# Performance work log

Measured on AMD Instinct MI355X. Metric: run time of the kernel, lower is better.

Reference implementation:

```python
import jax, jax.numpy as jnp
import numpy as np

B = 128
IN = 256
NLVL = 6
KLVL = 3
CH = 4
C = 4 * CH * CH          # 64 channels per node
OU = 8                   # out_filter_siz_u
OV = 8                   # out_filter_siz_v
NK = 2 ** KLVL           # 8 leaf nodes per axis
W_SCALE = 1.0 / 16.0     # ~1/sqrt(2*2*C) so 7 stacked relu-convs stay numerically sane


def setup_inputs() -> dict:
    key = jax.random.key(0)
    ks = jax.random.split(key, 2 * NLVL + 4)
    fx = IN // 2 ** NLVL  # 4: input patch filter size
    inp = {}
    inp["in_data"] = jax.random.normal(ks[0], (B, IN, IN, 1), jnp.float32)
    inp["in_filter"] = jax.random.normal(ks[1], (fx, fx, 1, C), jnp.float32) * W_SCALE
    inp["in_bias"] = jnp.zeros((C,), jnp.float32)
    i = 2
    for lvl in range(1, NLVL + 1):
        n = 2 ** min(lvl, KLVL)  # node grid: grows to 2^klvl then stays
        inp[f"f{lvl}"] = jax.random.normal(ks[i], (n, n, 2, 2, C, C), jnp.float32) * W_SCALE
        inp[f"b{lvl}"] = jnp.zeros((n, n, C), jnp.float32)
        i += 1
    inp["Wd"] = jax.random.normal(ks[i], (NK, NK, 2, C, OU * OV), jnp.float32) * W_SCALE
    return inp


def _node_conv(x, w, b):
    # x: [Nu,Nv,B,H,W,C]; w: [Nu,Nv,2,2,C,C]; 2x2 stride-2 VALID conv per node
    Nu, Nv, Bn, H, W, Cc = x.shape
    xr = x.reshape(Nu, Nv, Bn, H // 2, 2, W // 2, 2, Cc)
    y = jnp.einsum('uvbhxwyc,uvxyco->uvbhwo', xr, w)
    return jax.nn.relu(y + b[:, :, None, None, None, :])


def _forward(in_data, in_filter, in_bias, fs, bs, Wd):
    Bn = in_data.shape[0]
    fx, fy = in_filter.shape[0], in_filter.shape[1]
    # input interp conv: stride == kernel -> non-overlapping patch GEMM
    xr = in_data[..., 0].reshape(Bn, in_data.shape[1] // fx, fx, in_data.shape[2] // fy, fy)
    x = jax.nn.relu(jnp.einsum('bxpyq,pqc->bxyc', xr, in_filter[:, :, 0, :]) + in_bias)
    x = x[None, None]  # [1,1,B,2^nlvl,2^nlvl,C] node grid
    for lvl in range(1, NLVL + 1):
        if lvl <= KLVL:
            # children (itu,itv) read parent (itu//2, itv//2)
            x = jnp.repeat(jnp.repeat(x, 2, axis=0), 2, axis=1)
        x = _node_conv(x, fs[lvl - 1], bs[lvl - 1])
    feats = x[:, :, :, 0, 0, :]  # [NK,NK,B,C]; spatial is 1x1 at level nlvl
    out = jnp.einsum('uvbc,uvrck->uvbrk', feats, Wd)  # r in {real, imag}
    out = out.reshape(NK, NK, Bn, 2, OU, OV)
    out = jnp.transpose(out, (2, 0, 4, 1, 5, 3))  # [B,itu,ou,itv,ov,2]
    return out.reshape(Bn, NK * OU, NK * OV, 2)


def reference(in_data, in_filter, in_bias, f1, b1, f2, b2, f3, b3, f4, b4, f5, b5, f6, b6, Wd):
    fs = (f1, f2, f3, f4, f5, f6)
    bs = (b1, b2, b3, b4, b5, b6)
    return _forward(in_data, in_filter, in_bias, fs, bs, Wd)
```

## Files before the change

### kernel.cpp

```cpp
#include <hip/hip_runtime.h>
#include <hip/hip_bf16.h>
#include <cstdint>
#include <cstddef>


typedef __attribute__((ext_vector_type(8))) short short8;
typedef __attribute__((ext_vector_type(4))) float f32x4;
typedef unsigned short ushort_t;

static __device__ __forceinline__ float b2f(const __hip_bfloat16 x) {
    return __bfloat162float(x);
}
static __device__ __forceinline__ ushort_t f2bf(float x) {
    __hip_bfloat16 h = __float2bfloat16(x);
    ushort_t u;
    __builtin_memcpy(&u, &h, 2);
    return u;
}
static __device__ __forceinline__ void gl_lds16(const void* g, void* l) {
    __builtin_amdgcn_global_load_lds(
        (const __attribute__((address_space(1))) void*)g,
        (__attribute__((address_space(3))) void*)l, 16, 0, 0);
}
#define WAIT_LGKM0() __builtin_amdgcn_s_waitcnt(0xC07F)
#define WAIT_VM0()   __builtin_amdgcn_s_waitcnt(0x0F70)

__global__ __launch_bounds__(256) void k_prep(
    const uint32_t* __restrict__ in_words,
    const void* f1, const void* f2, const void* f3,
    const void* f4, const void* f5, const void* f6, const void* wdsrc,
    const void* b1, const void* b2, const void* b3,
    const void* b4, const void* b5, const void* b6,
    ushort_t* __restrict__ wbuf, ushort_t* __restrict__ wdbuf,
    float* __restrict__ bbuf, int* __restrict__ flag)
{
    __shared__ int sflag;
    const int t = threadIdx.x;
    if (t < 64) {
        const float v = __uint_as_float(in_words[t]);
        const bool plaus = (v == 0.0f) || (fabsf(v) > 1e-8f && fabsf(v) < 1e4f);
        const unsigned long long m = __ballot(plaus);
        if (t == 0) sflag = (__popcll(m) >= 48) ? 0 : 1;
    }
    __syncthreads();
    const int isbf = sflag;
    const int gid = blockIdx.x * 256 + t;
    if (blockIdx.x == 0 && t == 0) *flag = isbf;

    if (gid >= 648448) return;
    if (gid >= 630784) {
        const int bg = gid - 630784;
        const void* src; int base;
        if      (bg <   256) { src = b1; base = 0;     }
        else if (bg <  1280) { src = b2; base = 256;   }
        else if (bg <  5376) { src = b3; base = 1280;  }
        else if (bg <  9472) { src = b4; base = 5376;  }
        else if (bg < 13568) { src = b5; base = 9472;  }
        else                 { src = b6; base = 13568; }
        const int local = bg - base;
        bbuf[bg] = isbf ? b2f(((const __hip_bfloat16*)src)[local])
                        : ((const float*)src)[local];
        return;
    }
    if (gid >= 565248) {
        const int local = gid - 565248;
        const int lane = local & 63;
        const int slot = (local >> 6) & 15;
        const int site = local >> 10;
        const int ks2 = slot >> 3, nh = slot & 7, q = lane >> 4;
        const int n = nh * 16 + (lane & 15);
        const int r = n >> 6, kk = n & 63;
        const int cbase = ks2 * 32 + q * 8;
        ushort_t pk[8];
        if (isbf) {
            const ushort_t* s = (const ushort_t*)wdsrc;
            #pragma unroll
            for (int j = 0; j < 8; j++)
                pk[j] = s[(((size_t)(site * 2 + r) * 64 + cbase + j) * 64) + kk];
        } else {
            const float* s = (const float*)wdsrc;
            #pragma unroll
            for (int j = 0; j < 8; j++)
                pk[j] = f2bf(s[(((size_t)(site * 2 + r) * 64 + cbase + j) * 64) + kk]);
        }
        *(uint4*)&wdbuf[(size_t)local * 8] = *(uint4*)pk;
        return;
    }
    const void* fsrc; int base;
    if      (gid <   8192) { fsrc = f1; base = 0;      }
    else if (gid <  40960) { fsrc = f2; base = 8192;   }
    else if (gid < 172032) { fsrc = f3; base = 40960;  }
    else if (gid < 303104) { fsrc = f4; base = 172032; }
    else if (gid < 434176) { fsrc = f5; base = 303104; }
    else                   { fsrc = f6; base = 434176; }
    const int local = gid - base;
    const int lane = local & 63;
    const int slot = (local >> 6) & 7;
    const int sitetap = local >> 9;
    const int ks = slot >> 2, nh = slot & 3, q = lane >> 4;
    const int n = (lane & 15) + nh * 16;
    const int kbase = ks * 32 + q * 8;
    ushort_t pk[8];
    if (isbf) {
        const ushort_t* s = (const ushort_t*)fsrc + (size_t)sitetap * 4096;
        #pragma unroll
        for (int j = 0; j < 8; j++) pk[j] = s[(kbase + j) * 64 + n];
    } else {
        const float* s = (const float*)fsrc + (size_t)sitetap * 4096;
        #pragma unroll
        for (int j = 0; j < 8; j++) pk[j] = f2bf(s[(kbase + j) * 64 + n]);
    }
    *(uint4*)&wbuf[(size_t)gid * 8] = *(uint4*)pk;
}

__global__ __launch_bounds__(256) void k_stage0(
    const void* __restrict__ in_data, const void* __restrict__ filt,
    const void* __restrict__ bias, __hip_bfloat16* __restrict__ x0,
    const int* __restrict__ flag, int b_off)
{
    const int isbf = *flag;
    const int blk = blockIdx.x;
    const int X  = blk & 63;
    const int bl = blk >> 6;
    const int bg = bl + b_off;

    __shared__ float sIn[4][256];
    __shared__ float sF[16][64];
    __shared__ float sB[64];

    const int t = threadIdx.x;
    const size_t srow = ((size_t)bg * 256 + (size_t)X * 4) * 256;

    if (isbf) {
        const __hip_bfloat16* src = (const __hip_bfloat16*)in_data + srow;
        #pragma unroll
        for (int i = 0; i < 4; i++) {
            int flat = i * 256 + t;
            int p = flat >> 8, col = flat & 255;
            sIn[p][col] = b2f(src[(size_t)p * 256 + col]);
        }
        const __hip_bfloat16* fsrc = (const __hip_bfloat16*)filt;
        #pragma unroll
        for (int i = 0; i < 4; i++) {
            int flat = i * 256 + t;
            sF[flat >> 6][flat & 63] = b2f(fsrc[flat]);
        }
        if (t < 64) sB[t] = b2f(((const __hip_bfloat16*)bias)[t]);
    } else {
        const float* src = (const float*)in_data + srow;
        const int p = t >> 6, c4 = (t & 63) * 4;
        *(float4*)&sIn[p][c4] = *(const float4*)(src + (size_t)p * 256 + c4);
        const float* fsrc = (const float*)filt;
        #pragma unroll
        for (int i = 0; i < 4; i++) {
            int flat = i * 256 + t;
            sF[flat >> 6][flat & 63] = fsrc[flat];
        }
        if (t < 64) sB[t] = ((const float*)bias)[t];
    }
    __syncthreads();

    const int ty = t >> 4;
    const int tc = t & 15;

    float acc[4][4];
    {
        const float4 bv = *(const float4*)&sB[tc * 4];
        #pragma unroll
        for (int yi = 0; yi < 4; yi++) {
            acc[yi][0] = bv.x; acc[yi][1] = bv.y;
            acc[yi][2] = bv.z; acc[yi][3] = bv.w;
        }
    }

    #pragma unroll
    for (int p = 0; p < 4; p++) {
        float4 rin[4], rf[4];
        #pragma unroll
        for (int yi = 0; yi < 4; yi++)
            rin[yi] = *(const float4*)&sIn[p][ty * 16 + yi * 4];
        #pragma unroll
        for (int q = 0; q < 4; q++)
            rf[q] = *(const float4*)&sF[p * 4 + q][tc * 4];
        #pragma unroll
        for (int yi = 0; yi < 4; yi++) {
            #pragma unroll
            for (int q = 0; q < 4; q++) {
                const float a = ((const float*)&rin[yi])[q];
                acc[yi][0] = fmaf(a, rf[q].x, acc[yi][0]);
                acc[yi][1] = fmaf(a, rf[q].y, acc[yi][1]);
                acc[yi][2] = fmaf(a, rf[q].z, acc[yi][2]);
                acc[yi][3] = fmaf(a, rf[q].w, acc[yi][3]);
            }
        }
    }

    ushort_t* dst = (ushort_t*)(x0 + ((size_t)bl * 64 + X) * 64 * 64);
    #pragma unroll
    for (int yi = 0; yi < 4; yi++) {
        uint2 pk;
        pk.x = (uint32_t)f2bf(fmaxf(acc[yi][0], 0.f))
             | ((uint32_t)f2bf(fmaxf(acc[yi][1], 0.f)) << 16);
        pk.y = (uint32_t)f2bf(fmaxf(acc[yi][2], 0.f))
             | ((uint32_t)f2bf(fmaxf(acc[yi][3], 0.f)) << 16);
        *(uint2*)(dst + (size_t)(ty * 4 + yi) * 64 + tc * 4) = pk;
    }
}

__global__ __launch_bounds__(256) void k_level4(
    const __hip_bfloat16* __restrict__ xin,
    const ushort_t* __restrict__ wbuf,
    const float* __restrict__ bbuf,
    __hip_bfloat16* __restrict__ xout,
    int Nv_out, int HW, int Bc, int mtiles)
{
    __shared__ ushort_t smem[20480];
    __shared__ float sBias[4][64];
    ushort_t* sA = smem;
    ushort_t* sB = smem + 4096;

    int idx = blockIdx.x;
    const int mt = idx % mtiles; idx /= mtiles;
    const int w  = idx % HW; idx /= HW;
    const int h  = idx % HW; idx /= HW;
    const int Nv_in = Nv_out >> 1;
    const int vp = idx % Nv_in;
    const int up = idx / Nv_in;

    const int t = threadIdx.x;
    const int wave = t >> 6, lane = t & 63;
    const int lm = lane & 15, lq = lane >> 4;

    {
        const int ct = t >> 6, o = t & 63;
        const int so_t = (2 * up + (ct >> 1)) * Nv_out + (2 * vp + (ct & 1));
        sBias[ct][o] = bbuf[so_t * 64 + o];
    }

    const int so = (2 * up + (wave >> 1)) * Nv_out + (2 * vp + (wave & 1));
    const int H_in = HW * 2;
    const size_t bstride = (size_t)H_in * H_in * 64;
    const size_t siteb = (size_t)(up * Nv_in + vp) * Bc * bstride;
    const ushort_t* wsite = wbuf + (size_t)so * 4 * 4096;

    const f32x4 zero = {0.f, 0.f, 0.f, 0.f};
    f32x4 acc[4][4];
    #pragma unroll
    for (int i = 0; i < 4; i++)
        #pragma unroll
        for (int j = 0; j < 4; j++) acc[i][j] = zero;

    for (int tap = 0; tap < 4; tap++) {
        const int hi = 2 * h + (tap >> 1), wi = 2 * w + (tap & 1);
        const size_t tapoff = siteb + ((size_t)hi * H_in + wi) * 64;
        #pragma unroll
        for (int s2 = 0; s2 < 2; s2++) {
            const int s = wave * 2 + s2;
            const int ks = s >> 2, mh = s & 3;
            int b = mt * 64 + lm + mh * 16;
            if (b >= Bc) b = Bc - 1;
            gl_lds16(xin + tapoff + (size_t)b * bstride + ks * 32 + lq * 8,
                     &sA[s * 512]);
        }
        const ushort_t* wt = wsite + (size_t)tap * 4096;
        #pragma unroll
        for (int s = 0; s < 8; s++) {
            gl_lds16(wt + s * 512 + lane * 8, &sB[wave * 4096 + s * 512]);
        }
        __syncthreads();

        #pragma unroll
        for (int ks = 0; ks < 2; ks++) {
            short8 bf0 = *(const short8*)&sB[wave * 4096 + (ks * 4 + 0) * 512 + lane * 8];
            short8 bf1 = *(const short8*)&sB[wave * 4096 + (ks * 4 + 1) * 512 + lane * 8];
            short8 bf2 = *(const short8*)&sB[wave * 4096 + (ks * 4 + 2) * 512 + lane * 8];
            short8 bf3 = *(const short8*)&sB[wave * 4096 + (ks * 4 + 3) * 512 + lane * 8];
            #pragma unroll
            for (int fm = 0; fm < 4; fm++) {
                short8 a = *(const short8*)&sA[(ks * 4 + fm) * 512 + lane * 8];
                acc[fm][0] = __builtin_amdgcn_mfma_f32_16x16x32_bf16(a, bf0, acc[fm][0], 0, 0, 0);
                acc[fm][1] = __builtin_amdgcn_mfma_f32_16x16x32_bf16(a, bf1, acc[fm][1], 0, 0, 0);
                acc[fm][2] = __builtin_amdgcn_mfma_f32_16x16x32_bf16(a, bf2, acc[fm][2], 0, 0, 0);
                acc[fm][3] = __builtin_amdgcn_mfma_f32_16x16x32_bf16(a, bf3, acc[fm][3], 0, 0, 0);
            }
        }
        __syncthreads();
    }

    float bv[4];
    #pragma unroll
    for (int fn = 0; fn < 4; fn++) bv[fn] = sBias[wave][fn * 16 + lm];
    ushort_t* so_buf = smem + wave * 4352;
    #pragma unroll
    for (int fm = 0; fm < 4; fm++) {
        #pragma unroll
        for (int fn = 0; fn < 4; fn++) {
            #pragma unroll
            for (int r = 0; r < 4; r++) {
                const int row = fm * 16 + lq * 4 + r;
                so_buf[row * 68 + fn * 16 + lm] =
                    f2bf(fmaxf(acc[fm][fn][r] + bv[fn], 0.f));
            }
        }
    }
    __syncthreads();

    const size_t ostride = (size_t)HW * HW * 64;
    const size_t obase = (size_t)so * Bc * ostride + ((size_t)h * HW + w) * 64;
    #pragma unroll
    for (int i = 0; i < 8; i++) {
        const int task = i * 64 + lane;
        const int oct = task & 7, row = task >> 3;
        const int b = mt * 64 + row;
        if (b < Bc) {
            *(uint4*)(xout + obase + (size_t)b * ostride + oct * 8) =
                *(const uint4*)&so_buf[row * 68 + oct * 8];
        }
    }
}

__global__ __launch_bounds__(256, 1) void k_f456(
    const __hip_bfloat16* __restrict__ xin,
    const ushort_t* __restrict__ w4, const ushort_t* __restrict__ w5,
    const ushort_t* __restrict__ w6, const ushort_t* __restrict__ wd,
    const float* __restrict__ b4, const float* __restrict__ b5,
    const float* __restrict__ b6,
    void* __restrict__ out, const int* __restrict__ flag,
    int Bc, int b_off, int mtiles)
{
    const int isbf = *flag;
    const int bx = blockIdx.x;
    const int mt = bx % mtiles;
    const int site = bx / mtiles;
    const int u = site >> 3, v = site & 7;

    __shared__ ushort_t smem[74752];
    __shared__ float sBias[192];

    const int t = threadIdx.x;
    const int wv = t >> 6, lane = t & 63;
    const int lm = lane & 15, lq = lane >> 4;

    if (t < 64) {
        sBias[t]       = b4[site * 64 + t];
        sBias[64 + t]  = b5[site * 64 + t];
        sBias[128 + t] = b6[site * 64 + t];
    }

    {
        const ushort_t* w4s = w4 + (size_t)site * 16384;
        const ushort_t* w5s = w5 + (size_t)site * 16384;
        #pragma unroll
        for (int s2 = 0; s2 < 8; s2++) {
            const int s = wv * 8 + s2;
            gl_lds16(w4s + s * 512 + lane * 8, &smem[s * 512]);
            gl_lds16(w5s + s * 512 + lane * 8, &smem[16384 + s * 512]);
        }
    }
    __syncthreads();

    const f32x4 zero = {0.f, 0.f, 0.f, 0.f};
    const int h5 = wv >> 1, w5p = wv & 1;
    ushort_t* mid1w = smem + 32768 + wv * 8448;
    ushort_t* Aw = smem + 66560 + wv * 2048;
    const size_t sb = (size_t)site * Bc;

    for (int i = 0; i < 4; i++) {
        const int h4 = 2 * h5 + (i >> 1), w4p = 2 * w5p + (i & 1);
        f32x4 acc[2][4];
        #pragma unroll
        for (int a_ = 0; a_ < 2; a_++)
            #pragma unroll
            for (int b_ = 0; b_ < 4; b_++) acc[a_][b_] = zero;

        for (int tap = 0; tap < 4; tap++) {
            const int h3 = 2 * h4 + (tap >> 1), w3 = 2 * w4p + (tap & 1);
            WAIT_LGKM0();
            #pragma unroll
            for (int sl = 0; sl < 4; sl++) {
                const int ks = sl >> 1, mh = sl & 1;
                int b = mt * 32 + mh * 16 + lm;
                if (b >= Bc) b = Bc - 1;
                gl_lds16(xin + (sb + b) * 4096 + (h3 * 8 + w3) * 64 + ks * 32 + lq * 8,
                         &Aw[sl * 512]);
            }
            WAIT_VM0();
            #pragma unroll
            for (int ks = 0; ks < 2; ks++) {
                #pragma unroll
                for (int fm = 0; fm < 2; fm++) {
                    short8 a = *(const short8*)&Aw[(ks * 2 + fm) * 512 + lane * 8];
                    #pragma unroll
                    for (int fn = 0; fn < 4; fn++) {
                        short8 bfr = *(const short8*)&smem[(tap * 8 + ks * 4 + fn) * 512 + lane * 8];
                        acc[fm][fn] = __builtin_amdgcn_mfma_f32_16x16x32_bf16(a, bfr, acc[fm][fn], 0, 0, 0);
                    }
                }
            }
        }
        #pragma unroll
        for (int fm = 0; fm < 2; fm++) {
            #pragma unroll
            for (int fn = 0; fn < 4; fn++) {
                #pragma unroll
                for (int r = 0; r < 4; r++) {
                    const int m = fm * 16 + lq * 4 + r;
                    const int ch = fn * 16 + lm;
                    mid1w[m * 264 + i * 64 + ch] =
                        f2bf(fmaxf(acc[fm][fn][r] + sBias[ch], 0.f));
                }
            }
        }
    }

    {
        f32x4 acc2[2][4];
        #pragma unroll
        for (int a_ = 0; a_ < 2; a_++)
            #pragma unroll
            for (int b_ = 0; b_ < 4; b_++) acc2[a_][b_] = zero;

        #pragma unroll
        for (int i = 0; i < 4; i++) {
            #pragma unroll
            for (int ks = 0; ks < 2; ks++) {
                short8 a0 = *(const short8*)&mid1w[lm * 264 + i * 64 + ks * 32 + lq * 8];
                short8 a1 = *(const short8*)&mid1w[(16 + lm) * 264 + i * 64 + ks * 32 + lq * 8];
                #pragma unroll
                for (int fn = 0; fn < 4; fn++) {
                    short8 bfr = *(const short8*)&smem[16384 + (i * 8 + ks * 4 + fn) * 512 + lane * 8];
                    acc2[0][fn] = __builtin_amdgcn_mfma_f32_16x16x32_bf16(a0, bfr, acc2[0][fn], 0, 0, 0);
                    acc2[1][fn] = __builtin_amdgcn_mfma_f32_16x16x32_bf16(a1, bfr, acc2[1][fn], 0, 0, 0);
                }
            }
        }
        #pragma unroll
        for (int fm = 0; fm < 2; fm++) {
            #pragma unroll
            for (int fn = 0; fn < 4; fn++) {
                #pragma unroll
                for (int r = 0; r < 4; r++) {
                    const int m = fm * 16 + lq * 4 + r;
                    const int ch = fn * 16 + lm;
                    mid1w[m * 72 + ch] =
                        f2bf(fmaxf(acc2[fm][fn][r] + sBias[64 + ch], 0.f));
                }
            }
        }
    }
    __syncthreads();

    {
        const ushort_t* w6s = w6 + (size_t)site * 16384;
        const ushort_t* wds = wd + (size_t)site * 8192;
        #pragma unroll
        for (int s2 = 0; s2 < 8; s2++) {
            const int s = wv * 8 + s2;
            gl_lds16(w6s + s * 512 + lane * 8, &smem[s * 512]);
        }
        #pragma unroll
        for (int s2 = 0; s2 < 4; s2++) {
            const int s = wv * 4 + s2;
            gl_lds16(wds + s * 512 + lane * 8, &smem[16384 + s * 512]);
        }
    }
    __syncthreads();

    {
        f32x4 acc3[2];
        acc3[0] = zero; acc3[1] = zero;
        #pragma unroll
        for (int tap = 0; tap < 4; tap++) {
            const ushort_t* sl = smem + 32768 + tap * 8448;
            #pragma unroll
            for (int ks = 0; ks < 2; ks++) {
                short8 a0 = *(const short8*)&sl[lm * 72 + ks * 32 + lq * 8];
                short8 a1 = *(const short8*)&sl[(16 + lm) * 72 + ks * 32 + lq * 8];
                short8 bfr = *(const short8*)&smem[(tap * 8 + ks * 4 + wv) * 512 + lane * 8];
                acc3[0] = __builtin_amdgcn_mfma_f32_16x16x32_bf16(a0, bfr, acc3[0], 0, 0, 0);
                acc3[1] = __builtin_amdgcn_mfma_f32_16x16x32_bf16(a1, bfr, acc3[1], 0, 0, 0);
            }
        }
        ushort_t* mid3 = smem + 66560;
        #pragma unroll
        for (int fm = 0; fm < 2; fm++) {
            #pragma unroll
            for (int r = 0; r < 4; r++) {
                const int m = fm * 16 + lq * 4 + r;
                const int ch = wv * 16 + lm;
                mid3[m * 72 + ch] =
                    f2bf(fmaxf(acc3[fm][r] + sBias[128 + ch], 0.f));
            }
        }
    }
    __syncthreads();

    {
        const ushort_t* mid3 = smem + 66560;
        f32x4 acc4[2][2];
        acc4[0][0] = zero; acc4[0][1] = zero; acc4[1][0] = zero; acc4[1][1] = zero;
        #pragma unroll
        for (int ks = 0; ks < 2; ks++) {
            short8 a0 = *(const short8*)&mid3[lm * 72 + ks * 32 + lq * 8];
            short8 a1 = *(const short8*)&mid3[(16 + lm) * 72 + ks * 32 + lq * 8];
            #pragma unroll
            for (int n2 = 0; n2 < 2; n2++) {
                const int nh = 2 * wv + n2;
                short8 bfr = *(const short8*)&smem[16384 + (ks * 8 + nh) * 512 + lane * 8];
                acc4[0][n2] = __builtin_amdgcn_mfma_f32_16x16x32_bf16(a0, bfr, acc4[0][n2], 0, 0, 0);
                acc4[1][n2] = __builtin_amdgcn_mfma_f32_16x16x32_bf16(a1, bfr, acc4[1][n2], 0, 0, 0);
            }
        }
        #pragma unroll
        for (int fm = 0; fm < 2; fm++) {
            #pragma unroll
            for (int n2 = 0; n2 < 2; n2++) {
                const int n = (2 * wv + n2) * 16 + lm;
                const int rr = n >> 6, ou = (n >> 3) & 7, ov = n & 7;
                const size_t obase =
                    (((size_t)(u * 8 + ou)) * 64 + (v * 8 + ov)) * 2 + rr;
                #pragma unroll
                for (int reg = 0; reg < 4; reg++) {
                    const int brow = mt * 32 + fm * 16 + lq * 4 + reg;
                    if (brow < Bc) {
                        const size_t oidx = obase + (size_t)(b_off + brow) * 8192;
                        if (isbf) ((__hip_bfloat16*)out)[oidx] =
                            __float2bfloat16(acc4[fm][n2][reg]);
                        else ((float*)out)[oidx] = acc4[fm][n2][reg];
                    }
                }
            }
        }
    }
}

extern "C" void kernel_launch(void* const* d_in, const int* in_sizes, int n_in,
                              void* d_out, int out_size, void* d_ws, size_t ws_size,
                              hipStream_t stream)
{
    (void)in_sizes; (void)n_in; (void)out_size;

    const void* in_data = d_in[0];
    const void* filt    = d_in[1];
    const void* bias0   = d_in[2];
    const void* fl[7];
    const void* bl[7];
    for (int l = 1; l <= 6; l++) {
        fl[l] = d_in[1 + 2 * l];
        bl[l] = d_in[2 + 2 * l];
    }
    const void* Wd = d_in[15];

    const int Bfull = 128;
    const size_t perB = (size_t)64 * 64 * 64;

    const size_t wbufBytes  = 565248ull * 16;
    const size_t wdbufBytes = 65536ull * 16;
    const size_t bbufBytes  = 17664ull * 4;
    const size_t headBytes  = 256 + wbufBytes + wdbufBytes + bbufBytes;

    const size_t avail = ws_size > headBytes ? ws_size - headBytes : 0;
    int Bc = 0;
    for (int c = 128; c >= 1; c >>= 1) {
        if ((size_t)2 * c * perB * sizeof(__hip_bfloat16) <= avail) { Bc = c; break; }
    }
    if (Bc == 0) return;

    int* flag = (int*)d_ws;
    ushort_t* wbuf  = (ushort_t*)((char*)d_ws + 256);
    ushort_t* wdbuf = (ushort_t*)((char*)d_ws + 256 + wbufBytes);
    float* bbuf = (float*)((char*)d_ws + 256 + wbufBytes + wdbufBytes);
    __hip_bfloat16* bufA = (__hip_bfloat16*)((char*)d_ws + headBytes);
    __hip_bfloat16* bufB = bufA + (size_t)Bc * perB;

    static const size_t w_off[7] = {0, 0, 65536, 327680, 1376256, 2424832, 3473408};
    static const int    b_off_tab[7] = {0, 0, 256, 1280, 5376, 9472, 13568};

    k_prep<<<dim3(2533), 256, 0, stream>>>(
        (const uint32_t*)in_data,
        fl[1], fl[2], fl[3], fl[4], fl[5], fl[6], Wd,
        bl[1], bl[2], bl[3], bl[4], bl[5], bl[6],
        wbuf, wdbuf, bbuf, flag);

    const int mt4 = (Bc + 63) / 64;
    const int mt32 = (Bc + 31) / 32;

    for (int b_off = 0; b_off < Bfull; b_off += Bc) {
        k_stage0<<<dim3(Bc * 64), 256, 0, stream>>>(in_data, filt, bias0, bufA, flag, b_off);

        __hip_bfloat16* cur = bufA;
        __hip_bfloat16* nxt = bufB;
        for (int lvl = 1; lvl <= 3; lvl++) {
            const int Nu = 1 << lvl;
            const int H  = 64 >> lvl;
            const int Nv_in = Nu >> 1;
            dim3 grid(Nv_in * Nv_in * H * H * mt4);
            k_level4<<<grid, 256, 0, stream>>>(cur, wbuf + w_off[lvl],
                bbuf + b_off_tab[lvl], nxt, Nu, H, Bc, mt4);
            __hip_bfloat16* tmp = cur; cur = nxt; nxt = tmp;
        }

        k_f456<<<dim3(64 * mt32), 256, 0, stream>>>(cur,
            wbuf + w_off[4], wbuf + w_off[5], wbuf + w_off[6], wdbuf,
            bbuf + b_off_tab[4], bbuf + b_off_tab[5], bbuf + b_off_tab[6],
            d_out, flag, Bc, b_off, mt32);
    }
}
```

Before: 248.8 us.

## Fuse input patch conv with level-1 node conv into one kernel

Replaces the separate stage-0 kernel and the first level-1 launch with a single kernel. It computes the input patch convolution for a 2x2 neighbourhood of 32 batch items in registers, writes the bf16 result straight into LDS in MFMA fragment layout, then runs the level-1 2x2 conv with MFMA against weights streamed into LDS. This removes the global write and re-read of the large stage-0 activation buffer and one launch, at the cost of more LDS per block and recomputing the FP32 patch GEMM per tile.

```diff
diff --git a/kernel.cpp b/kernel.cpp
--- a/kernel.cpp
+++ b/kernel.cpp
@@ -113,97 +113,169 @@
     *(uint4*)&wbuf[(size_t)gid * 8] = *(uint4*)pk;
 }
 
-__global__ __launch_bounds__(256) void k_stage0(
-    const void* __restrict__ in_data, const void* __restrict__ filt,
-    const void* __restrict__ bias, __hip_bfloat16* __restrict__ x0,
-    const int* __restrict__ flag, int b_off)
+__global__ __launch_bounds__(256, 2) void k_s01(
+    const void* __restrict__ in_data,
+    const void* __restrict__ filt,
+    const void* __restrict__ bias0,
+    const ushort_t* __restrict__ w1,
+    const float* __restrict__ b1,
+    __hip_bfloat16* __restrict__ xout,
+    const int* __restrict__ flag, int Bc, int b_off, int mtiles)
 {
     const int isbf = *flag;
-    const int blk = blockIdx.x;
-    const int X  = blk & 63;
-    const int bl = blk >> 6;
-    const int bg = bl + b_off;
-
-    __shared__ float sIn[4][256];
+    int idx = blockIdx.x;
+    const int mt = idx % mtiles; idx /= mtiles;
+    const int w = idx & 31;
+    const int h = idx >> 5;
+
+    __shared__ float sIn[32][64];
     __shared__ float sF[16][64];
-    __shared__ float sB[64];
+    __shared__ float sB0[64];
+    __shared__ float sBias[4][64];
+    __shared__ ushort_t sA[4 * 4 * 512];
+    __shared__ ushort_t sB[4 * 8 * 512];
 
     const int t = threadIdx.x;
-    const size_t srow = ((size_t)bg * 256 + (size_t)X * 4) * 256;
+    const int wave = t >> 6, lane = t & 63;
+    const int lm = lane & 15, lq = lane >> 4;
 
     if (isbf) {
-        const __hip_bfloat16* src = (const __hip_bfloat16*)in_data + srow;
-        #pragma unroll
-        for (int i = 0; i < 4; i++) {
-            int flat = i * 256 + t;
-            int p = flat >> 8, col = flat & 255;
-            sIn[p][col] = b2f(src[(size_t)p * 256 + col]);
-        }
         const __hip_bfloat16* fsrc = (const __hip_bfloat16*)filt;
         #pragma unroll
         for (int i = 0; i < 4; i++) {
             int flat = i * 256 + t;
             sF[flat >> 6][flat & 63] = b2f(fsrc[flat]);
         }
-        if (t < 64) sB[t] = b2f(((const __hip_bfloat16*)bias)[t]);
+        if (t < 64) sB0[t] = b2f(((const __hip_bfloat16*)bias0)[t]);
     } else {
-        const float* src = (const float*)in_data + srow;
-        const int p = t >> 6, c4 = (t & 63) * 4;
-        *(float4*)&sIn[p][c4] = *(const float4*)(src + (size_t)p * 256 + c4);
         const float* fsrc = (const float*)filt;
         #pragma unroll
         for (int i = 0; i < 4; i++) {
             int flat = i * 256 + t;
             sF[flat >> 6][flat & 63] = fsrc[flat];
         }
-        if (t < 64) sB[t] = ((const float*)bias)[t];
-    }
-    __syncthreads();
-
-    const int ty = t >> 4;
-    const int tc = t & 15;
-
-    float acc[4][4];
-    {
-        const float4 bv = *(const float4*)&sB[tc * 4];
-        #pragma unroll
-        for (int yi = 0; yi < 4; yi++) {
-            acc[yi][0] = bv.x; acc[yi][1] = bv.y;
-            acc[yi][2] = bv.z; acc[yi][3] = bv.w;
-        }
-    }
+        if (t < 64) sB0[t] = ((const float*)bias0)[t];
+    }
+    sBias[t >> 6][t & 63] = b1[(t >> 6) * 64 + (t & 63)];
 
     #pragma unroll
-    for (int p = 0; p < 4; p++) {
-        float4 rin[4], rf[4];
-        #pragma unroll
-        for (int yi = 0; yi < 4; yi++)
-            rin[yi] = *(const float4*)&sIn[p][ty * 16 + yi * 4];
-        #pragma unroll
-        for (int q = 0; q < 4; q++)
-            rf[q] = *(const float4*)&sF[p * 4 + q][tc * 4];
-        #pragma unroll
-        for (int yi = 0; yi < 4; yi++) {
-            #pragma unroll
-            for (int q = 0; q < 4; q++) {
-                const float a = ((const float*)&rin[yi])[q];
-                acc[yi][0] = fmaf(a, rf[q].x, acc[yi][0]);
-                acc[yi][1] = fmaf(a, rf[q].y, acc[yi][1]);
-                acc[yi][2] = fmaf(a, rf[q].z, acc[yi][2]);
-                acc[yi][3] = fmaf(a, rf[q].w, acc[yi][3]);
-            }
-        }
-    }
-
-    ushort_t* dst = (ushort_t*)(x0 + ((size_t)bl * 64 + X) * 64 * 64);
+    for (int i = 0; i < 2; i++) {
+        const int task = i * 256 + t;
+        const int half = task & 1, r = (task >> 1) & 7, b = task >> 4;
+        int bl = mt * 32 + b;
+        if (bl >= Bc) bl = Bc - 1;
+        const size_t off = ((size_t)(b_off + bl) * 256 + 8 * h + r) * 256
+                         + 8 * w + half * 4;
+        float4 val;
+        if (isbf) {
+            const __hip_bfloat16* s = (const __hip_bfloat16*)in_data + off;
+            val.x = b2f(s[0]); val.y = b2f(s[1]); val.z = b2f(s[2]); val.w = b2f(s[3]);
+        } else {
+            val = *(const float4*)((const float*)in_data + off);
+        }
+        *(float4*)&sIn[b][r * 8 + half * 4] = val;
+    }
+    __syncthreads();
+
+    {
+        const int vb = t >> 3, oct = t & 7;
+        float4 pf[16][2];
+        #pragma unroll
+        for (int pq = 0; pq < 16; pq++) {
+            pf[pq][0] = *(const float4*)&sF[pq][oct * 8];
+            pf[pq][1] = *(const float4*)&sF[pq][oct * 8 + 4];
+        }
+        const int ks = oct >> 2;
+        const int slot = ks * 2 + (vb >> 4);
+        const int ln = (vb & 15) | ((oct & 3) << 4);
+        #pragma unroll
+        for (int tap = 0; tap < 4; tap++) {
+            const int x = tap >> 1, y = tap & 1;
+            float4 rin[4];
+            #pragma unroll
+            for (int p = 0; p < 4; p++)
+                rin[p] = *(const float4*)&sIn[vb][(4 * x + p) * 8 + 4 * y];
+            float acc8[8];
+            #pragma unroll
+            for (int j = 0; j < 8; j++) acc8[j] = sB0[oct * 8 + j];
+            #pragma unroll
+            for (int p = 0; p < 4; p++) {
+                #pragma unroll
+                for (int q = 0; q < 4; q++) {
+                    const float a = ((const float*)&rin[p])[q];
+                    const float* fp = (const float*)&pf[p * 4 + q][0];
+                    #pragma unroll
+                    for (int j = 0; j < 8; j++)
+                        acc8[j] = fmaf(a, fp[j], acc8[j]);
+                }
+            }
+            ushort_t pk[8];
+            #pragma unroll
+            for (int j = 0; j < 8; j++) pk[j] = f2bf(fmaxf(acc8[j], 0.f));
+            *(uint4*)&sA[((tap * 4 + slot) * 64 + ln) * 8] = *(uint4*)pk;
+        }
+    }
+    __syncthreads();
+
+    const f32x4 zero = {0.f, 0.f, 0.f, 0.f};
+    f32x4 accm[2][4];
     #pragma unroll
-    for (int yi = 0; yi < 4; yi++) {
-        uint2 pk;
-        pk.x = (uint32_t)f2bf(fmaxf(acc[yi][0], 0.f))
-             | ((uint32_t)f2bf(fmaxf(acc[yi][1], 0.f)) << 16);
-        pk.y = (uint32_t)f2bf(fmaxf(acc[yi][2], 0.f))
-             | ((uint32_t)f2bf(fmaxf(acc[yi][3], 0.f)) << 16);
-        *(uint2*)(dst + (size_t)(ty * 4 + yi) * 64 + tc * 4) = pk;
+    for (int i = 0; i < 2; i++)
+        #pragma unroll
+        for (int j = 0; j < 4; j++) accm[i][j] = zero;
+
+    const ushort_t* wsite = w1 + (size_t)wave * 4 * 4096;
+    for (int tap = 0; tap < 4; tap++) {
+        WAIT_LGKM0();
+        const ushort_t* wt = wsite + (size_t)tap * 4096;
+        #pragma unroll
+        for (int s = 0; s < 8; s++)
+            gl_lds16(wt + s * 512 + lane * 8, &sB[wave * 4096 + s * 512]);
+        WAIT_VM0();
+        #pragma unroll
+        for (int ks = 0; ks < 2; ks++) {
+            #pragma unroll
+            for (int fm = 0; fm < 2; fm++) {
+                short8 a = *(const short8*)&sA[((tap * 4 + ks * 2 + fm) * 64 + lane) * 8];
+                #pragma unroll
+                for (int fn = 0; fn < 4; fn++) {
+                    short8 bfr = *(const short8*)&sB[wave * 4096 + (ks * 4 + fn) * 512 + lane * 8];
+                    accm[fm][fn] = __builtin_amdgcn_mfma_f32_16x16x32_bf16(a, bfr, accm[fm][fn], 0, 0, 0);
+                }
+            }
+        }
+    }
+
+    WAIT_LGKM0();
+    {
+        float bv[4];
+        #pragma unroll
+        for (int fn = 0; fn < 4; fn++) bv[fn] = sBias[wave][fn * 16 + lm];
+        ushort_t* ob = &sB[wave * 4096];
+        #pragma unroll
+        for (int fm = 0; fm < 2; fm++) {
+            #pragma unroll
+            for (int fn = 0; fn < 4; fn++) {
+                #pragma unroll
+                for (int r = 0; r < 4; r++) {
+                    const int row = fm * 16 + lq * 4 + r;
+                    ob[row * 68 + fn * 16 + lm] =
+                        f2bf(fmaxf(accm[fm][fn][r] + bv[fn], 0.f));
+                }
+            }
+        }
+        const size_t ostride = (size_t)32 * 32 * 64;
+        const size_t obase = (size_t)wave * Bc * ostride + ((size_t)h * 32 + w) * 64;
+        #pragma unroll
+        for (int i = 0; i < 4; i++) {
+            const int task = i * 64 + lane;
+            const int oc = task & 7, row = task >> 3;
+            const int b = mt * 32 + row;
+            if (b < Bc) {
+                *(uint4*)(xout + obase + (size_t)b * ostride + oc * 8) =
+                    *(const uint4*)&ob[row * 68 + oc * 8];
+            }
+        }
     }
 }
 
@@ -586,11 +658,13 @@
     const int mt32 = (Bc + 31) / 32;
 
     for (int b_off = 0; b_off < Bfull; b_off += Bc) {
-        k_stage0<<<dim3(Bc * 64), 256, 0, stream>>>(in_data, filt, bias0, bufA, flag, b_off);
+        k_s01<<<dim3(1024 * mt32), 256, 0, stream>>>(
+            in_data, filt, bias0, wbuf + w_off[1], bbuf + b_off_tab[1],
+            bufA, flag, Bc, b_off, mt32);
 
         __hip_bfloat16* cur = bufA;
         __hip_bfloat16* nxt = bufB;
-        for (int lvl = 1; lvl <= 3; lvl++) {
+        for (int lvl = 2; lvl <= 3; lvl++) {
             const int Nu = 1 << lvl;
             const int H  = 64 >> lvl;
             const int Nv_in = Nu >> 1;
```

Result: slower. 271.5 us (+9.1%).

## Fuse tree levels 2 and 3 into one kernel via LDS intermediate

Applied to the files above, without the earlier changes.

Adds a kernel that computes level-2 node convolutions for four sibling nodes and immediately feeds the results, held in shared memory, into the level-3 convolutions. The level-2 activation no longer makes a round trip through global memory, and one launch is removed per batch chunk. The cost is that each block recomputes for a 32-batch tile using up to four waves, with a different grid decomposition and occupancy target, which may lower MFMA efficiency or occupancy compared with the generic level kernel.

```diff
diff --git a/kernel.cpp b/kernel.cpp
--- a/kernel.cpp
+++ b/kernel.cpp
@@ -319,6 +319,169 @@
     }
 }
 
+__global__ __launch_bounds__(256, 4) void k_L23(
+    const __hip_bfloat16* __restrict__ xin,
+    const ushort_t* __restrict__ w2buf,
+    const ushort_t* __restrict__ w3buf,
+    const float* __restrict__ b2, const float* __restrict__ b3,
+    __hip_bfloat16* __restrict__ xout,
+    int Bc, int mtiles)
+{
+    __shared__ ushort_t smem[17408];
+    __shared__ float sBias2[64];
+    __shared__ float sBias3[4][64];
+
+    int idx = blockIdx.x;
+    const int sib = idx & 3; idx >>= 2;
+    const int mt = idx % mtiles; idx /= mtiles;
+    const int hw = idx & 63; idx >>= 6;
+    const int s1 = idx;
+    const int h3 = hw >> 3, w3 = hw & 7;
+    const int u2 = 2 * (s1 >> 1) + (sib >> 1);
+    const int v2 = 2 * (s1 & 1) + (sib & 1);
+    const int s2 = u2 * 4 + v2;
+
+    const int t = threadIdx.x;
+    const int wv = t >> 6, lane = t & 63;
+    const int lm = lane & 15, lq = lane >> 4;
+
+    {
+        const int ct = t >> 6, o = t & 63;
+        const int s3t = (2 * u2 + (ct >> 1)) * 8 + 2 * v2 + (ct & 1);
+        sBias3[ct][o] = b3[s3t * 64 + o];
+        if (t < 64) sBias2[t] = b2[s2 * 64 + t];
+    }
+    __syncthreads();
+
+    const f32x4 zero = {0.f, 0.f, 0.f, 0.f};
+    ushort_t* Aw = smem + wv * 2048;
+    ushort_t* midw = smem + 8192 + wv * 2304;
+
+    {
+        const int h2 = 2 * h3 + (wv >> 1), w2p = 2 * w3 + (wv & 1);
+        const size_t a1base = (size_t)s1 * Bc * 65536;
+        const ushort_t* w2site = w2buf + (size_t)s2 * 16384;
+
+        f32x4 acc[2][4];
+        #pragma unroll
+        for (int a_ = 0; a_ < 2; a_++)
+            #pragma unroll
+            for (int b_ = 0; b_ < 4; b_++) acc[a_][b_] = zero;
+
+        for (int tap = 0; tap < 4; tap++) {
+            const int hi = 2 * h2 + (tap >> 1), wi = 2 * w2p + (tap & 1);
+            WAIT_LGKM0();
+            #pragma unroll
+            for (int sl = 0; sl < 4; sl++) {
+                const int ks = sl >> 1, mh = sl & 1;
+                int b = mt * 32 + mh * 16 + lm;
+                if (b >= Bc) b = Bc - 1;
+                gl_lds16(xin + a1base + (size_t)b * 65536
+                             + ((size_t)hi * 32 + wi) * 64 + ks * 32 + lq * 8,
+                         &Aw[sl * 512]);
+            }
+            short8 bfr[2][4];
+            #pragma unroll
+            for (int ks = 0; ks < 2; ks++)
+                #pragma unroll
+                for (int fn = 0; fn < 4; fn++)
+                    bfr[ks][fn] = *(const short8*)(w2site + (size_t)tap * 4096
+                                                   + (ks * 4 + fn) * 512 + lane * 8);
+            WAIT_VM0();
+            #pragma unroll
+            for (int ks = 0; ks < 2; ks++) {
+                #pragma unroll
+                for (int fm = 0; fm < 2; fm++) {
+                    short8 a = *(const short8*)&Aw[(ks * 2 + fm) * 512 + lane * 8];
+                    #pragma unroll
+                    for (int fn = 0; fn < 4; fn++)
+                        acc[fm][fn] = __builtin_amdgcn_mfma_f32_16x16x32_bf16(
+                            a, bfr[ks][fn], acc[fm][fn], 0, 0, 0);
+                }
+            }
+        }
+        #pragma unroll
+        for (int fm = 0; fm < 2; fm++) {
+            #pragma unroll
+            for (int fn = 0; fn < 4; fn++) {
+                #pragma unroll
+                for (int r = 0; r < 4; r++) {
+                    const int m = fm * 16 + lq * 4 + r;
+                    const int ch = fn * 16 + lm;
+                    midw[m * 72 + ch] =
+                        f2bf(fmaxf(acc[fm][fn][r] + sBias2[ch], 0.f));
+                }
+            }
+        }
+    }
+    __syncthreads();
+
+    f32x4 acc3[2][4];
+    #pragma unroll
+    for (int a_ = 0; a_ < 2; a_++)
+        #pragma unroll
+        for (int b_ = 0; b_ < 4; b_++) acc3[a_][b_] = zero;
+
+    const int u3 = 2 * u2 + (wv >> 1), v3 = 2 * v2 + (wv & 1);
+    const int s3 = u3 * 8 + v3;
+    {
+        const ushort_t* w3site = w3buf + (size_t)s3 * 16384;
+        for (int tap = 0; tap < 4; tap++) {
+            const ushort_t* sl = smem + 8192 + tap * 2304;
+            short8 bfr[2][4];
+            #pragma unroll
+            for (int ks = 0; ks < 2; ks++)
+                #pragma unroll
+                for (int fn = 0; fn < 4; fn++)
+                    bfr[ks][fn] = *(const short8*)(w3site + (size_t)tap * 4096
+                                                   + (ks * 4 + fn) * 512 + lane * 8);
+            #pragma unroll
+            for (int ks = 0; ks < 2; ks++) {
+                short8 a0 = *(const short8*)&sl[lm * 72 + ks * 32 + lq * 8];
+                short8 a1 = *(const short8*)&sl[(16 + lm) * 72 + ks * 32 + lq * 8];
+                #pragma unroll
+                for (int fn = 0; fn < 4; fn++) {
+                    acc3[0][fn] = __builtin_amdgcn_mfma_f32_16x16x32_bf16(
+                        a0, bfr[ks][fn], acc3[0][fn], 0, 0, 0);
+                    acc3[1][fn] = __builtin_amdgcn_mfma_f32_16x16x32_bf16(
+                        a1, bfr[ks][fn], acc3[1][fn], 0, 0, 0);
+                }
+            }
+        }
+    }
+    __syncthreads();
+
+    {
+        float bv[4];
+        #pragma unroll
+        for (int fn = 0; fn < 4; fn++) bv[fn] = sBias3[wv][fn * 16 + lm];
+        ushort_t* epi = midw;
+        #pragma unroll
+        for (int fm = 0; fm < 2; fm++) {
+            #pragma unroll
+            for (int fn = 0; fn < 4; fn++) {
+                #pragma unroll
+                for (int r = 0; r < 4; r++) {
+                    const int row = fm * 16 + lq * 4 + r;
+                    epi[row * 68 + fn * 16 + lm] =
+                        f2bf(fmaxf(acc3[fm][fn][r] + bv[fn], 0.f));
+                }
+            }
+        }
+        const size_t obase = (size_t)s3 * Bc * 4096 + ((size_t)h3 * 8 + w3) * 64;
+        #pragma unroll
+        for (int i = 0; i < 4; i++) {
+            const int task = i * 64 + lane;
+            const int oc = task & 7, row = task >> 3;
+            const int b = mt * 32 + row;
+            if (b < Bc) {
+                *(uint4*)(xout + obase + (size_t)b * 4096 + oc * 8) =
+                    *(const uint4*)&epi[row * 68 + oc * 8];
+            }
+        }
+    }
+}
+
 __global__ __launch_bounds__(256, 1) void k_f456(
     const __hip_bfloat16* __restrict__ xin,
     const ushort_t* __restrict__ w4, const ushort_t* __restrict__ w5,
@@ -588,19 +751,14 @@
     for (int b_off = 0; b_off < Bfull; b_off += Bc) {
         k_stage0<<<dim3(Bc * 64), 256, 0, stream>>>(in_data, filt, bias0, bufA, flag, b_off);
 
-        __hip_bfloat16* cur = bufA;
-        __hip_bfloat16* nxt = bufB;
-        for (int lvl = 1; lvl <= 3; lvl++) {
-            const int Nu = 1 << lvl;
-            const int H  = 64 >> lvl;
-            const int Nv_in = Nu >> 1;
-            dim3 grid(Nv_in * Nv_in * H * H * mt4);
-            k_level4<<<grid, 256, 0, stream>>>(cur, wbuf + w_off[lvl],
-                bbuf + b_off_tab[lvl], nxt, Nu, H, Bc, mt4);
-            __hip_bfloat16* tmp = cur; cur = nxt; nxt = tmp;
-        }
-
-        k_f456<<<dim3(64 * mt32), 256, 0, stream>>>(cur,
+        k_level4<<<dim3(32 * 32 * mt4), 256, 0, stream>>>(
+            bufA, wbuf + w_off[1], bbuf + b_off_tab[1], bufB, 2, 32, Bc, mt4);
+
+        k_L23<<<dim3(1024 * mt32), 256, 0, stream>>>(
+            bufB, wbuf + w_off[2], wbuf + w_off[3],
+            bbuf + b_off_tab[2], bbuf + b_off_tab[3], bufA, Bc, mt32);
+
+        k_f456<<<dim3(64 * mt32), 256, 0, stream>>>(bufA,
             wbuf + w_off[4], wbuf + w_off[5], wbuf + w_off[6], wdbuf,
             bbuf + b_off_tab[4], bbuf + b_off_tab[5], bbuf + b_off_tab[6],
             d_out, flag, Bc, b_off, mt32);
```

After: 259.3 us. 4.2% more time.

## Double-buffer activation tiles and load weights directly to registers in level-4 kernel

Applied to the files above, without the earlier changes.

The level-4 node conv kernel now keeps two activation buffers in LDS. It prefetches the next tap's activations while the MFMAs for the current tap run, and needs one barrier per tap instead of two. Weight fragments are read straight from global memory into registers instead of being staged through LDS, which also shrinks the shared memory footprint. In exchange, global weight loads now sit on the critical path of each tap, and register pressure goes up.

```diff
diff --git a/kernel.cpp b/kernel.cpp
--- a/kernel.cpp
+++ b/kernel.cpp
@@ -214,10 +214,8 @@
     __hip_bfloat16* __restrict__ xout,
     int Nv_out, int HW, int Bc, int mtiles)
 {
-    __shared__ ushort_t smem[20480];
+    __shared__ ushort_t smem[17408];
     __shared__ float sBias[4][64];
-    ushort_t* sA = smem;
-    ushort_t* sB = smem + 4096;
 
     int idx = blockIdx.x;
     const int mt = idx % mtiles; idx /= mtiles;
@@ -243,6 +241,15 @@
     const size_t siteb = (size_t)(up * Nv_in + vp) * Bc * bstride;
     const ushort_t* wsite = wbuf + (size_t)so * 4 * 4096;
 
+    int arow[2];
+    #pragma unroll
+    for (int s2 = 0; s2 < 2; s2++) {
+        const int s = wave * 2 + s2;
+        int b = mt * 64 + lm + (s & 3) * 16;
+        if (b >= Bc) b = Bc - 1;
+        arow[s2] = b;
+    }
+
     const f32x4 zero = {0.f, 0.f, 0.f, 0.f};
     f32x4 acc[4][4];
     #pragma unroll
@@ -250,41 +257,51 @@
         #pragma unroll
         for (int j = 0; j < 4; j++) acc[i][j] = zero;
 
-    for (int tap = 0; tap < 4; tap++) {
-        const int hi = 2 * h + (tap >> 1), wi = 2 * w + (tap & 1);
-        const size_t tapoff = siteb + ((size_t)hi * H_in + wi) * 64;
+    {
+        const size_t tapoff = siteb + ((size_t)(2 * h) * H_in + (2 * w)) * 64;
         #pragma unroll
         for (int s2 = 0; s2 < 2; s2++) {
             const int s = wave * 2 + s2;
-            const int ks = s >> 2, mh = s & 3;
-            int b = mt * 64 + lm + mh * 16;
-            if (b >= Bc) b = Bc - 1;
-            gl_lds16(xin + tapoff + (size_t)b * bstride + ks * 32 + lq * 8,
-                     &sA[s * 512]);
-        }
-        const ushort_t* wt = wsite + (size_t)tap * 4096;
-        #pragma unroll
-        for (int s = 0; s < 8; s++) {
-            gl_lds16(wt + s * 512 + lane * 8, &sB[wave * 4096 + s * 512]);
+            gl_lds16(xin + tapoff + (size_t)arow[s2] * bstride + (s >> 2) * 32 + lq * 8,
+                     &smem[s * 512]);
+        }
+    }
+    __syncthreads();
+
+    int cur = 0;
+    for (int tap = 0; tap < 4; tap++) {
+        short8 bfr[2][4];
+        #pragma unroll
+        for (int ks = 0; ks < 2; ks++)
+            #pragma unroll
+            for (int fn = 0; fn < 4; fn++)
+                bfr[ks][fn] = *(const short8*)(wsite + (size_t)tap * 4096
+                                               + (ks * 4 + fn) * 512 + lane * 8);
+        if (tap < 3) {
+            const int nt = tap + 1;
+            const int hi = 2 * h + (nt >> 1), wi = 2 * w + (nt & 1);
+            const size_t tapoff = siteb + ((size_t)hi * H_in + wi) * 64;
+            #pragma unroll
+            for (int s2 = 0; s2 < 2; s2++) {
+                const int s = wave * 2 + s2;
+                gl_lds16(xin + tapoff + (size_t)arow[s2] * bstride + (s >> 2) * 32 + lq * 8,
+                         &smem[(cur ^ 1) * 4096 + s * 512]);
+            }
+        }
+
+        #pragma unroll
+        for (int ks = 0; ks < 2; ks++) {
+            #pragma unroll
+            for (int fm = 0; fm < 4; fm++) {
+                short8 a = *(const short8*)&smem[cur * 4096 + (ks * 4 + fm) * 512 + lane * 8];
+                acc[fm][0] = __builtin_amdgcn_mfma_f32_16x16x32_bf16(a, bfr[ks][0], acc[fm][0], 0, 0, 0);
+                acc[fm][1] = __builtin_amdgcn_mfma_f32_16x16x32_bf16(a, bfr[ks][1], acc[fm][1], 0, 0, 0);
+                acc[fm][2] = __builtin_amdgcn_mfma_f32_16x16x32_bf16(a, bfr[ks][2], acc[fm][2], 0, 0, 0);
+                acc[fm][3] = __builtin_amdgcn_mfma_f32_16x16x32_bf16(a, bfr[ks][3], acc[fm][3], 0, 0, 0);
+            }
         }
         __syncthreads();
-
-        #pragma unroll
-        for (int ks = 0; ks < 2; ks++) {
-            short8 bf0 = *(const short8*)&sB[wave * 4096 + (ks * 4 + 0) * 512 + lane * 8];
-            short8 bf1 = *(const short8*)&sB[wave * 4096 + (ks * 4 + 1) * 512 + lane * 8];
-            short8 bf2 = *(const short8*)&sB[wave * 4096 + (ks * 4 + 2) * 512 + lane * 8];
-            short8 bf3 = *(const short8*)&sB[wave * 4096 + (ks * 4 + 3) * 512 + lane * 8];
-            #pragma unroll
-            for (int fm = 0; fm < 4; fm++) {
-                short8 a = *(const short8*)&sA[(ks * 4 + fm) * 512 + lane * 8];
-                acc[fm][0] = __builtin_amdgcn_mfma_f32_16x16x32_bf16(a, bf0, acc[fm][0], 0, 0, 0);
-                acc[fm][1] = __builtin_amdgcn_mfma_f32_16x16x32_bf16(a, bf1, acc[fm][1], 0, 0, 0);
-                acc[fm][2] = __builtin_amdgcn_mfma_f32_16x16x32_bf16(a, bf2, acc[fm][2], 0, 0, 0);
-                acc[fm][3] = __builtin_amdgcn_mfma_f32_16x16x32_bf16(a, bf3, acc[fm][3], 0, 0, 0);
-            }
-        }
-        __syncthreads();
+        cur ^= 1;
     }
 
     float bv[4];
```

Result: slower. 258.1 us (+3.7%).
